# Kernel optimization log

Measured on AMD Instinct MI355X. Metric: run time of the kernel, lower is better.

Reference implementation:

```python
import jax, jax.numpy as jnp
import numpy as np

N_NODES = 65536
N_FEAT = 64
N_EDGES = 1048576
N_GRAPHS = 16
LP_ITERS = 30


def setup_inputs() -> dict:
    key = jax.random.key(0)
    k1, k2, k3 = jax.random.split(key, 3)
    x = jax.random.normal(k1, (N_NODES, N_FEAT), dtype=jnp.float32)
    edge_index = jax.random.randint(k2, (2, N_EDGES), 0, N_NODES, dtype=jnp.int32)
    batch = jnp.sort(jax.random.randint(k3, (N_NODES,), 0, N_GRAPHS, dtype=jnp.int32))
    v2 = jnp.full((1,), 3.5, dtype=jnp.float32)  # learnable affinity scale param
    return {"x": x, "edge_index": edge_index, "batch": batch, "v2": v2}


def _lp_clustering(row, col, aff, n_nodes, n_iters):
    """Label propagation: each node adopts the neighbor label with max summed affinity."""
    E = row.shape[0]
    aff = jax.lax.stop_gradient(aff)  # clustering is discrete, no grad path

    def body(_, labels):
        lab_c = labels[col]                                    # neighbor labels per edge
        order = jnp.lexsort((lab_c, row))                      # sort by (row, neighbor-label)
        r_s, l_s, w_s = row[order], lab_c[order], aff[order]
        new_grp = jnp.concatenate([jnp.ones((1,), bool),
                                   (r_s[1:] != r_s[:-1]) | (l_s[1:] != l_s[:-1])])
        gid = jnp.cumsum(new_grp) - 1                          # dense (row,label) group ids
        gsum = jax.ops.segment_sum(w_s, gid, num_segments=E)   # affinity mass per group
        gcnt = jax.ops.segment_sum(jnp.ones_like(w_s), gid, num_segments=E)
        valid = gcnt > 0
        g_row = jnp.where(valid, jax.ops.segment_max(r_s, gid, num_segments=E), 0)
        g_lab = jnp.where(valid, jax.ops.segment_max(l_s, gid, num_segments=E), n_nodes)
        node_max = jax.ops.segment_max(jnp.where(valid, gsum, -jnp.inf), g_row,
                                       num_segments=n_nodes)
        win = valid & (gsum == node_max[g_row])
        # smallest winning label == torch argmax first-hit tie-break
        return jax.ops.segment_min(jnp.where(win, g_lab, n_nodes), g_row,
                                   num_segments=n_nodes)

    labels0 = jnp.arange(n_nodes, dtype=row.dtype)
    return jax.lax.fori_loop(0, n_iters, body, labels0)


def _forward(x, edge_index, batch, v2):
    n = x.shape[0]
    loops = jnp.arange(n, dtype=edge_index.dtype)
    ei = jnp.concatenate([edge_index, jnp.stack([loops, loops])], axis=1)  # add_self_loops
    row, col = ei[0], ei[1]

    # P2-style affinities: log_aff = -v2 * ||x_i - x_j||^2 ; forward exponentiates
    sqdist = jnp.sum((x[row] - x[col]) ** 2, axis=1)  # [E]
    losses = jnp.mean(sqdist)
    aff = jnp.exp(-v2[0] * sqdist)

    node_labels = _lp_clustering(row, col, aff, n, LP_ITERS)

    # unique(return_inverse): dense relabel of surviving cluster ids (sorted order)
    present = jnp.zeros((n,), jnp.int32).at[node_labels].set(1)
    cluster_labels = (jnp.cumsum(present) - 1)[node_labels]

    # max_pool_x: scatter-max node features into clusters (padded to n rows)
    cx = jax.ops.segment_max(x, cluster_labels, num_segments=n)
    cb = jax.ops.segment_max(batch, cluster_labels, num_segments=n)
    nonempty = jax.ops.segment_sum(jnp.ones((n,), jnp.int32), cluster_labels,
                                   num_segments=n) > 0
    cx = jnp.where(nonempty[:, None], cx, 0.0)
    cb = jnp.where(nonempty, cb, -1)

    # coalesce(cluster_labels[edge_index]): sort + dedupe, duplicates padded with -1
    mr, mc = cluster_labels[row], cluster_labels[col]
    order = jnp.lexsort((mc, mr))
    mr_s, mc_s = mr[order], mc[order]
    dup = jnp.concatenate([jnp.zeros((1,), bool),
                           (mr_s[1:] == mr_s[:-1]) & (mc_s[1:] == mc_s[:-1])])
    cei = jnp.stack([jnp.where(dup, -1, mr_s), jnp.where(dup, -1, mc_s)])

    return cx, cei, cb, cluster_labels, losses


def reference(x, edge_index, batch, v2):
    return _forward(x, edge_index, batch, v2)
```

## Files before the change

### kernel.cpp

```cpp
#include <hip/hip_runtime.h>
#include <hip/hip_fp16.h>
#include <hip/hip_cooperative_groups.h>

namespace cg = cooperative_groups;

#define DI __device__ __forceinline__

constexpr int NN   = 65536;
constexpr int NF   = 64;
constexpr int E0c  = 1048576;
constexpr int ET   = E0c + NN;
constexpr int LPITERS = 30;
constexpr int KPOS = 16;
constexpr int MSCH = 4096;
constexpr int NCHK = ET / MSCH;
constexpr int SCAP = 8192;
constexpr int CAP0 = 6144;
constexpr int BPB  = CAP0 / 64;
constexpr int NPART2 = 256 * BPB;

constexpr int O_CX   = 0;
constexpr int O_CEI0 = NN * NF;
constexpr int O_CEI1 = O_CEI0 + ET;
constexpr int O_CB   = O_CEI0 + 2 * ET;
constexpr int O_CL   = O_CB + NN;
constexpr int O_LOSS = O_CL + NN;

constexpr int W_CHG   = 0;
constexpr int W_NCLUS = 32;
constexpr int W_H1    = 64;
constexpr int W_GC0   = W_H1 + 256;
constexpr int W_GC1   = W_GC0 + 256;
constexpr int W_SCP   = 832;
constexpr int W_SCO   = W_SCP + 256;
constexpr int W_PART  = W_SCO + 256;
constexpr int W_PCNT  = W_PART + NPART2;
constexpr int W_PCOL  = W_PCNT + NN;
constexpr int W_PW    = W_PCOL + NN*KPOS;
constexpr int W_L0    = W_PW + NN*KPOS;
constexpr int W_L1    = W_L0 + NN;
constexpr int W_PRES  = W_L1 + NN;
constexpr int W_PSUM  = W_PRES + NN;
constexpr int W_CLU   = W_PSUM + NN;
constexpr int W_CBA   = W_CLU + NN;
constexpr int W_K0    = W_CBA + NN;
constexpr int W_K1    = W_K0 + 256*CAP0;

DI void edge_rc(const int* ei, int e, int& r, int& c) {
  if (e < E0c) { r = ei[e]; c = ei[E0c + e]; }
  else         { r = e - E0c; c = r; }
}

DI unsigned fenc(float f) {
  unsigned u = __float_as_uint(f);
  return (u & 0x80000000u) ? ~u : (u | 0x80000000u);
}
DI float fdec(unsigned u) {
  u = (u & 0x80000000u) ? (u & 0x7fffffffu) : ~u;
  return __uint_as_float(u);
}

DI int lp_step(int r, int d, int c0, int c1, float q0, float q1,
               const int* __restrict__ pcol, const float* __restrict__ pw,
               const int* __restrict__ lin) {
  int bl = NN;
  if (d == 1) {
    bl = lin[c0];
  } else if (d == 2) {
    int l0 = lin[c0], l1 = lin[c1];
    if (l0 == l1) bl = l0;
    else if (q1 > q0 || (q1 == q0 && l1 < l0)) bl = l1;
    else bl = l0;
  } else if (d > 2) {
    float best = 0.f;
    for (int i = 0; i < d; ++i) {
      int li = lin[pcol[r * KPOS + i]];
      bool dup = false;
      for (int j = 0; j < i; ++j)
        if (lin[pcol[r * KPOS + j]] == li) { dup = true; break; }
      if (dup) continue;
      float sum = 0.f;
      for (int j = i; j < d; ++j)
        if (lin[pcol[r * KPOS + j]] == li) sum += pw[r * KPOS + j];
      if (sum > best || (sum == best && li < bl)) { best = sum; bl = li; }
    }
  }
  return bl;
}


__global__ __launch_bounds__(256) void init_small(int* ws) {
  for (int i = threadIdx.x; i < 832; i += 256) ws[i] = 0;
}

__global__ __launch_bounds__(256) void emultisplit(const int* __restrict__ ei,
                                                   int* __restrict__ gcur0,
                                                   unsigned* __restrict__ K0,
                                                   int* __restrict__ pcnt,
                                                   int* __restrict__ L0,
                                                   const float2* __restrict__ x2,
                                                   unsigned* __restrict__ xh) {
  __shared__ unsigned skey[MSCH];
  __shared__ unsigned short binid[MSCH];
  __shared__ int hl[256], ss[256], hs[256], hc[256], gb[256];
  int t = threadIdx.x;
  if (blockIdx.x < 256) {
    int rr = blockIdx.x * 256 + t;
    pcnt[rr] = 0;
    L0[rr] = rr;
  }
  for (int i = blockIdx.x * 256 + t; i < NN * NF / 2; i += NCHK * 256) {
    float2 f = x2[i];
    __half2 h = __floats2half2_rn(f.x, f.y);
    xh[i] = *reinterpret_cast<unsigned*>(&h);
  }
  hl[t] = 0; __syncthreads();
  int base = blockIdx.x * MSCH;
  unsigned mykey[MSCH / 256];
  #pragma unroll
  for (int k = 0; k < MSCH / 256; ++k) {
    int e = base + k * 256 + t;
    int r, c; edge_rc(ei, e, r, c);
    unsigned key = ((unsigned)r << 16) | (unsigned)c;
    mykey[k] = key;
    atomicAdd(&hl[key >> 24], 1);
  }
  __syncthreads();
  int v = hl[t];
  ss[t] = v; __syncthreads();
  for (int off = 1; off < 256; off <<= 1) {
    int u = (t >= off) ? ss[t - off] : 0;
    __syncthreads();
    ss[t] += u;
    __syncthreads();
  }
  int excl = ss[t] - v;
  hs[t] = excl;
  hc[t] = excl;
  gb[t] = t * CAP0 + ((v > 0) ? atomicAdd(&gcur0[t], v) : 0);
  for (int j = excl; j < excl + v; ++j) binid[j] = (unsigned short)t;
  __syncthreads();
  #pragma unroll
  for (int k = 0; k < MSCH / 256; ++k) {
    int b = mykey[k] >> 24;
    int slot = atomicAdd(&hc[b], 1);
    skey[slot] = mykey[k];
  }
  __syncthreads();
  for (int i = t; i < MSCH; i += 256) {
    int b = binid[i];
    int pos = gb[b] + (i - hs[b]);
    if (pos < (b + 1) * CAP0) K0[pos] = skey[i];
  }
}

__global__ __launch_bounds__(256) void edge_pos2(const unsigned* __restrict__ xh,
                                                 const unsigned* __restrict__ K0,
                                                 const int* __restrict__ gcur0,
                                                 const float* __restrict__ v2,
                                                 float* __restrict__ part,
                                                 int* __restrict__ pcnt,
                                                 int* __restrict__ pcol,
                                                 float* __restrict__ pw) {
  __shared__ float ls[32];
  int t = threadIdx.x, grp = t >> 3, lane = t & 7;
  int bkt = blockIdx.x / BPB;
  int off = (blockIdx.x % BPB) * 64;
  int cnt = gcur0[bkt];
  if (off >= cnt) {
    if (t == 0) part[blockIdx.x] = 0.f;
    return;
  }
  float w = v2[0];
  unsigned kk[2]; bool act[2];
  uint4 A[2], B[2];
  #pragma unroll
  for (int q = 0; q < 2; ++q) {
    int j = off + grp * 2 + q;
    act[q] = (j < cnt);
    kk[q] = K0[bkt * CAP0 + (act[q] ? j : 0)];
  }
  #pragma unroll
  for (int q = 0; q < 2; ++q) {
    int r = kk[q] >> 16, c = kk[q] & 0xFFFF;
    A[q] = ((const uint4*)(xh + (size_t)r * 32))[lane];
    B[q] = ((const uint4*)(xh + (size_t)c * 32))[lane];
  }
  __builtin_amdgcn_sched_barrier(0);
  float lsum = 0.f;
  #pragma unroll
  for (int q = 0; q < 2; ++q) {
    const __half2* ah = reinterpret_cast<const __half2*>(&A[q]);
    const __half2* bh = reinterpret_cast<const __half2*>(&B[q]);
    __half2 d0 = __hsub2(ah[0], bh[0]);
    __half2 acc = __hmul2(d0, d0);
    __half2 d1 = __hsub2(ah[1], bh[1]); acc = __hfma2(d1, d1, acc);
    __half2 d2 = __hsub2(ah[2], bh[2]); acc = __hfma2(d2, d2, acc);
    __half2 d3 = __hsub2(ah[3], bh[3]); acc = __hfma2(d3, d3, acc);
    float s = __low2float(acc) + __high2float(acc);
    s += __shfl_xor(s, 1, 8);
    s += __shfl_xor(s, 2, 8);
    s += __shfl_xor(s, 4, 8);
    if (lane == 0 && act[q]) {
      int r = kk[q] >> 16, c = kk[q] & 0xFFFF;
      if (r == c) s = 0.f;
      lsum += s;
      float aff = expf(-w * s);
      if (aff > 0.f) {
        int slot = atomicAdd(&pcnt[r], 1);
        if (slot < KPOS) { pcol[r * KPOS + slot] = c; pw[r * KPOS + slot] = aff; }
      }
    }
  }
  if (lane == 0) ls[grp] = lsum;
  __syncthreads();
  if (t == 0) {
    float s = 0.f;
    #pragma unroll
    for (int k = 0; k < 32; ++k) s += ls[k];
    part[blockIdx.x] = s;
  }
}

__global__ __launch_bounds__(256) void lp_iter0(const int* __restrict__ pcnt,
                                                const int* __restrict__ pcol,
                                                const float* __restrict__ pw,
                                                const int* __restrict__ L0,
                                                int* __restrict__ L1,
                                                int* __restrict__ chg,
                                                const float* __restrict__ part,
                                                float* __restrict__ out_loss) {
  __shared__ float smf[256];
  int t = threadIdx.x;
  int r = blockIdx.x * 256 + t;
  int d = pcnt[r];
  if (d > KPOS) d = KPOS;
  int c0 = 0, c1 = 0; float q0 = 0.f, q1 = 0.f;
  if (d >= 1) { c0 = pcol[r * KPOS];     q0 = pw[r * KPOS]; }
  if (d >= 2) { c1 = pcol[r * KPOS + 1]; q1 = pw[r * KPOS + 1]; }
  int bl = lp_step(r, d, c0, c1, q0, q1, pcol, pw, L0);
  L1[r] = bl;
  if (bl != L0[r]) atomicOr(&chg[0], 1);
  if (blockIdx.x == 0) {
    float s = 0.f;
    for (int i = t; i < NPART2; i += 256) s += part[i];
    smf[t] = s; __syncthreads();
    for (int off = 128; off; off >>= 1) {
      if (t < off) smf[t] += smf[t + off];
      __syncthreads();
    }
    if (t == 0) out_loss[0] = smf[0] / (float)ET;
  }
}

__global__ __launch_bounds__(256) void general_tail(
    const int* __restrict__ pcnt, const int* __restrict__ pcol,
    const float* __restrict__ pw, int* __restrict__ L0, int* __restrict__ L1,
    int* __restrict__ chg, int* __restrict__ pres, int* __restrict__ psum,
    int* __restrict__ clu, float* __restrict__ out_cl, int* __restrict__ cba,
    unsigned* __restrict__ cxacc, const float* __restrict__ x,
    const int* __restrict__ batch, int* __restrict__ nclus_g,
    int* __restrict__ scp, int* __restrict__ sco, int* __restrict__ h1,
    const int* __restrict__ gcur0, int* __restrict__ gcur1,
    const unsigned* __restrict__ K0, unsigned* __restrict__ K1,
    float* __restrict__ out_cb) {
  if (chg[0] == 0) return;
  __shared__ int sm[256], hl[256], bases[256];
  __shared__ int sbc;
  cg::grid_group grid = cg::this_grid();
  int t = threadIdx.x, b = blockIdx.x;
  int r = b * 256 + t;
  pres[r] = 0;
  cba[r] = -1;
  {
    uint4 z = make_uint4(0u, 0u, 0u, 0u);
    uint4* p = (uint4*)(cxacc + ((size_t)r << 6));
    #pragma unroll
    for (int q = 0; q < 16; ++q) p[q] = z;
  }
  int mylab = L1[r];
  int d = pcnt[r]; if (d > KPOS) d = KPOS;
  int c0 = 0, c1 = 0; float q0 = 0.f, q1 = 0.f;
  if (d >= 1) { c0 = pcol[r * KPOS];     q0 = pw[r * KPOS]; }
  if (d >= 2) { c1 = pcol[r * KPOS + 1]; q1 = pw[r * KPOS + 1]; }
  for (int it = 1; it < LPITERS; ++it) {
    const int* lin = (it & 1) ? L1 : L0;
    int* lout = (it & 1) ? L0 : L1;
    int bl = lp_step(r, d, c0, c1, q0, q1, pcol, pw, lin);
    lout[r] = bl;
    if (bl != mylab) atomicOr(&chg[it], 1);
    mylab = bl;
    grid.sync();
    if (t == 0) sbc = *(volatile int*)&chg[it];
    __syncthreads();
    if (sbc == 0) break;
  }
  L0[r] = mylab;
  grid.sync();
  pres[mylab] = 1;
  grid.sync();
  int v = pres[r];
  sm[t] = v; __syncthreads();
  for (int off = 1; off < 256; off <<= 1) {
    int u = (t >= off) ? sm[t - off] : 0;
    __syncthreads();
    sm[t] += u;
    __syncthreads();
  }
  int lexcl = sm[t] - v;
  if (t == 255) scp[b] = sm[255];
  grid.sync();
  if (b == 0) {
    int p = scp[t];
    sm[t] = p; __syncthreads();
    for (int off = 1; off < 256; off <<= 1) {
      int u = (t >= off) ? sm[t - off] : 0;
      __syncthreads();
      sm[t] += u;
      __syncthreads();
    }
    sco[t] = sm[t] - p;
    if (t == 255) nclus_g[0] = sm[255];
  }
  grid.sync();
  psum[r] = lexcl + sco[b];
  grid.sync();
  int cr = psum[mylab];
  clu[r] = cr;
  out_cl[r] = (float)cr;
  grid.sync();
  for (int f = 0; f < 64; ++f)
    atomicMax(&cxacc[((size_t)cr << 6) + f], fenc(x[((size_t)r << 6) + f]));
  atomicMax(&cba[cr], batch[r]);
  grid.sync();
  int ncl = nclus_g[0];
  for (int f = 0; f < 64; ++f) {
    unsigned u = cxacc[((size_t)r << 6) + f];
    ((float*)cxacc)[((size_t)r << 6) + f] = (r < ncl) ? fdec(u) : 0.f;
  }
  out_cb[r] = (float)cba[r];
  hl[t] = 0; __syncthreads();
  int cnt = gcur0[b];
  for (int i = t; i < cnt; i += 256) {
    unsigned k = K0[b * CAP0 + i];
    atomicAdd(&hl[((unsigned)clu[k >> 16]) >> 8], 1);
  }
  __syncthreads();
  if (hl[t]) atomicAdd(&h1[t], hl[t]);
  grid.sync();
  int hv = h1[t];
  sm[t] = hv; __syncthreads();
  for (int off = 1; off < 256; off <<= 1) {
    int u = (t >= off) ? sm[t - off] : 0;
    __syncthreads();
    sm[t] += u;
    __syncthreads();
  }
  bases[t] = sm[t] - hv;
  __syncthreads();
  for (int i = t; i < cnt; i += 256) {
    unsigned k = K0[b * CAP0 + i];
    unsigned k1 = ((unsigned)clu[k >> 16] << 16) | (unsigned)clu[k & 0xFFFF];
    int b1 = k1 >> 24;
    int pos = bases[b1] + atomicAdd(&gcur1[b1], 1);
    K1[pos] = k1;
  }
}

__global__ __launch_bounds__(512) void sortwrite(unsigned* __restrict__ K0,
                                                 const int* __restrict__ gcur0,
                                                 unsigned* __restrict__ K1,
                                                 const int* __restrict__ h1,
                                                 const int* __restrict__ chg,
                                                 const float4* __restrict__ x4,
                                                 const int* __restrict__ batch,
                                                 float4* __restrict__ out_cx4,
                                                 float* __restrict__ out_cl,
                                                 float* __restrict__ out_cb,
                                                 float* __restrict__ o0,
                                                 float* __restrict__ o1) {
  __shared__ unsigned sk[SCAP];
  __shared__ int hl[256], ss[256], sbs[257], cur[256], sh[2];
  int t = threadIdx.x, b = blockIdx.x;
  bool fast = (chg[0] == 0);
  if (fast) {
    int base4 = b * (256 * 16);
    for (int i = t; i < 256 * 16; i += 512) out_cx4[base4 + i] = x4[base4 + i];
    int rbase = b * 256;
    for (int i = t; i < 256; i += 512) {
      out_cl[rbase + i] = (float)(rbase + i);
      out_cb[rbase + i] = (float)batch[rbase + i];
    }
  }
  const int* cnts = fast ? gcur0 : h1;
  if (t < 256) ss[t] = cnts[t];
  __syncthreads();
  for (int off = 1; off < 256; off <<= 1) {
    int u = (t < 256 && t >= off) ? ss[t - off] : 0;
    __syncthreads();
    if (t < 256) ss[t] += u;
    __syncthreads();
  }
  if (t == 0) { sh[0] = ss[b] - cnts[b]; sh[1] = cnts[b]; }
  __syncthreads();
  int sout = sh[0], d = sh[1];
  if (d <= 0) return;
  unsigned* kp = fast ? (K0 + b * CAP0) : (K1 + sout);
  if (d <= SCAP) {
    if (t < 256) hl[t] = 0;
    __syncthreads();
    for (int i = t; i < d; i += 512)
      atomicAdd(&hl[(kp[i] >> 16) & 0xFF], 1);
    __syncthreads();
    if (t < 256) ss[t] = hl[t];
    __syncthreads();
    for (int off = 1; off < 256; off <<= 1) {
      int u = (t < 256 && t >= off) ? ss[t - off] : 0;
      __syncthreads();
      if (t < 256) ss[t] += u;
      __syncthreads();
    }
    if (t < 256) { sbs[t] = ss[t] - hl[t]; cur[t] = ss[t] - hl[t]; }
    if (t == 255) sbs[256] = d;
    __syncthreads();
    for (int i = t; i < d; i += 512) {
      unsigned k = kp[i];
      int slot = atomicAdd(&cur[(k >> 16) & 0xFF], 1);
      sk[slot] = k;
    }
    __syncthreads();
    int wave = t >> 6, lane = t & 63;
    for (int sb = wave; sb < 256; sb += 8) {
      int s0 = sbs[sb], s1 = sbs[sb + 1], dd = s1 - s0;
      if (dd <= 1) continue;
      if (dd <= 64) {
        unsigned k = (lane < dd) ? sk[s0 + lane] : 0xFFFFFFFFu;
        #pragma unroll
        for (int size = 2; size <= 64; size <<= 1) {
          #pragma unroll
          for (int stride = size >> 1; stride > 0; stride >>= 1) {
            unsigned o = __shfl_xor(k, stride, 64);
            bool takeMin = (((lane & stride) == 0) == ((lane & size) == 0));
            unsigned mn = k < o ? k : o, mx = k < o ? o : k;
            k = takeMin ? mn : mx;
          }
        }
        if (lane < dd) sk[s0 + lane] = k;
      } else if (lane == 0) {
        for (int i = s0 + 1; i < s1; ++i) {
          unsigned k = sk[i];
          int j = i - 1;
          while (j >= s0 && sk[j] > k) { sk[j + 1] = sk[j]; --j; }
          sk[j + 1] = k;
        }
      }
    }
    __syncthreads();
    for (int i = t; i < d; i += 512) {
      unsigned k = sk[i];
      bool dup = (i > 0) && (sk[i - 1] == k);
      o0[sout + i] = dup ? -1.f : (float)(k >> 16);
      o1[sout + i] = dup ? -1.f : (float)(k & 0xffffu);
    }
  } else {
    if (t == 0) {
      for (int i = 1; i < d; ++i) {
        unsigned k = kp[i];
        int j = i - 1;
        while (j >= 0 && kp[j] > k) { kp[j + 1] = kp[j]; --j; }
        kp[j + 1] = k;
      }
    }
    __syncthreads();
    for (int i = t; i < d; i += 512) {
      unsigned k = kp[i];
      bool dup = (i > 0) && (kp[i - 1] == k);
      o0[sout + i] = dup ? -1.f : (float)(k >> 16);
      o1[sout + i] = dup ? -1.f : (float)(k & 0xffffu);
    }
  }
}


extern "C" void kernel_launch(void* const* d_in, const int* in_sizes, int n_in,
                              void* d_out, int out_size, void* d_ws, size_t ws_size,
                              hipStream_t stream) {
  const float* x   = (const float*)d_in[0];
  const int* ei    = (const int*)d_in[1];
  const int* batch = (const int*)d_in[2];
  const float* v2  = (const float*)d_in[3];
  float* out = (float*)d_out;
  int* ws = (int*)d_ws;
  unsigned* cxacc = (unsigned*)(out + O_CX);
  unsigned* xh = cxacc;

  init_small<<<1, 256, 0, stream>>>(ws);

  emultisplit<<<NCHK, 256, 0, stream>>>(ei, ws + W_GC0, (unsigned*)(ws + W_K0),
                                        ws + W_PCNT, ws + W_L0,
                                        (const float2*)x, xh);

  edge_pos2<<<NPART2, 256, 0, stream>>>(xh, (const unsigned*)(ws + W_K0),
                                        ws + W_GC0, v2, (float*)(ws + W_PART),
                                        ws + W_PCNT, ws + W_PCOL, (float*)(ws + W_PW));

  lp_iter0<<<NN / 256, 256, 0, stream>>>(ws + W_PCNT, ws + W_PCOL,
                                         (const float*)(ws + W_PW),
                                         ws + W_L0, ws + W_L1, ws + W_CHG,
                                         (const float*)(ws + W_PART), out + O_LOSS);

  {
    const int* pcnt = ws + W_PCNT;
    const int* pcol = ws + W_PCOL;
    const float* pw = (const float*)(ws + W_PW);
    int* L0 = ws + W_L0;
    int* L1 = ws + W_L1;
    int* chg = ws + W_CHG;
    int* pres = ws + W_PRES;
    int* psum = ws + W_PSUM;
    int* clu = ws + W_CLU;
    float* out_cl = out + O_CL;
    int* cba = ws + W_CBA;
    unsigned* cxa = cxacc;
    const float* x_ = x;
    const int* batch_ = batch;
    int* nclus_g = ws + W_NCLUS;
    int* scp = ws + W_SCP;
    int* sco = ws + W_SCO;
    int* h1 = ws + W_H1;
    const int* gcur0 = ws + W_GC0;
    int* gcur1 = ws + W_GC1;
    const unsigned* K0 = (const unsigned*)(ws + W_K0);
    unsigned* K1 = (unsigned*)(ws + W_K1);
    float* out_cb = out + O_CB;
    void* args[] = { (void*)&pcnt, (void*)&pcol, (void*)&pw,
                     (void*)&L0, (void*)&L1, (void*)&chg, (void*)&pres,
                     (void*)&psum, (void*)&clu, (void*)&out_cl, (void*)&cba,
                     (void*)&cxa, (void*)&x_, (void*)&batch_, (void*)&nclus_g,
                     (void*)&scp, (void*)&sco, (void*)&h1, (void*)&gcur0,
                     (void*)&gcur1, (void*)&K0, (void*)&K1, (void*)&out_cb };
    hipLaunchCooperativeKernel((const void*)general_tail, dim3(NN / 256),
                               dim3(256), args, 0, stream);
  }

  sortwrite<<<256, 512, 0, stream>>>((unsigned*)(ws + W_K0), ws + W_GC0,
                                     (unsigned*)(ws + W_K1), ws + W_H1,
                                     ws + W_CHG, (const float4*)x, batch,
                                     (float4*)(out + O_CX), out + O_CL,
                                     out + O_CB, out + O_CEI0, out + O_CEI1);
}
```

Measured before the change: 157.6 us.

## Split sortwrite into fast and general kernels, four blocks per bucket

Splits the final sort-and-write kernel into a fast-path kernel that runs 1024 blocks, with each block handling a quarter of a bucket's 256 sub-buckets, and a separate general-path kernel that exits early when the fast path applies. Each fast block builds the full bucket histogram on its own but scatters and sorts only its sub-bucket range. Sub-buckets of up to 64 keys are sorted with a wave-level bitonic sort using shuffles. The goal is more parallelism and better occupancy on the tail kernel, at the cost of re-reading each bucket's keys four times and one extra kernel launch.

```diff
diff --git a/kernel.cpp b/kernel.cpp
--- a/kernel.cpp
+++ b/kernel.cpp
@@ -367,33 +367,113 @@
   }
 }
 
-__global__ __launch_bounds__(512) void sortwrite(unsigned* __restrict__ K0,
-                                                 const int* __restrict__ gcur0,
-                                                 unsigned* __restrict__ K1,
-                                                 const int* __restrict__ h1,
-                                                 const int* __restrict__ chg,
-                                                 const float4* __restrict__ x4,
-                                                 const int* __restrict__ batch,
-                                                 float4* __restrict__ out_cx4,
-                                                 float* __restrict__ out_cl,
-                                                 float* __restrict__ out_cb,
-                                                 float* __restrict__ o0,
-                                                 float* __restrict__ o1) {
+__global__ __launch_bounds__(512) void sortwrite_fast(
+    const unsigned* __restrict__ K0, const int* __restrict__ gcur0,
+    const int* __restrict__ chg, const float4* __restrict__ x4,
+    const int* __restrict__ batch, float4* __restrict__ out_cx4,
+    float* __restrict__ out_cl, float* __restrict__ out_cb,
+    float* __restrict__ o0, float* __restrict__ o1) {
+  if (chg[0] != 0) return;
+  __shared__ unsigned sk[CAP0];
+  __shared__ int hl[256], ss[256], sbs[257], cur[256], sh[2];
+  int t = threadIdx.x;
+  int b = blockIdx.x >> 2, spl = blockIdx.x & 3;
+  {
+    int base4 = blockIdx.x * 1024;
+    for (int i = t; i < 1024; i += 512) out_cx4[base4 + i] = x4[base4 + i];
+    int rbase = blockIdx.x * 64;
+    for (int i = t; i < 64; i += 512) {
+      out_cl[rbase + i] = (float)(rbase + i);
+      out_cb[rbase + i] = (float)batch[rbase + i];
+    }
+  }
+  int cntb = gcur0[b];
+  if (cntb > CAP0) cntb = CAP0;
+  if (t < 256) ss[t] = gcur0[t];
+  __syncthreads();
+  for (int off = 1; off < 256; off <<= 1) {
+    int u = (t < 256 && t >= off) ? ss[t - off] : 0;
+    __syncthreads();
+    if (t < 256) ss[t] += u;
+    __syncthreads();
+  }
+  if (t == 0) sh[0] = ss[b] - gcur0[b];
+  if (t < 256) hl[t] = 0;
+  __syncthreads();
+  for (int i = t; i < cntb; i += 512)
+    atomicAdd(&hl[(K0[b * CAP0 + i] >> 16) & 0xFF], 1);
+  __syncthreads();
+  if (t < 256) ss[t] = hl[t];
+  __syncthreads();
+  for (int off = 1; off < 256; off <<= 1) {
+    int u = (t < 256 && t >= off) ? ss[t - off] : 0;
+    __syncthreads();
+    if (t < 256) ss[t] += u;
+    __syncthreads();
+  }
+  if (t < 256) { sbs[t] = ss[t] - hl[t]; cur[t] = ss[t] - hl[t]; }
+  if (t == 255) sbs[256] = cntb;
+  __syncthreads();
+  int sout_b = sh[0];
+  int sb0 = spl * 64, sb1 = sb0 + 64;
+  int mybase = sbs[sb0], myend = sbs[sb1];
+  if (myend <= mybase) return;
+  for (int i = t; i < cntb; i += 512) {
+    unsigned k = K0[b * CAP0 + i];
+    int sb = (k >> 16) & 0xFF;
+    if (sb >= sb0 && sb < sb1) {
+      int slot = atomicAdd(&cur[sb], 1);
+      sk[slot - mybase] = k;
+    }
+  }
+  __syncthreads();
+  int wave = t >> 6, lane = t & 63;
+  for (int sb = sb0 + wave; sb < sb1; sb += 8) {
+    int s0 = sbs[sb] - mybase, s1 = sbs[sb + 1] - mybase, dd = s1 - s0;
+    if (dd <= 1) continue;
+    if (dd <= 64) {
+      unsigned k = (lane < dd) ? sk[s0 + lane] : 0xFFFFFFFFu;
+      int P = (dd <= 16) ? 16 : ((dd <= 32) ? 32 : 64);
+      for (int size = 2; size <= P; size <<= 1) {
+        bool upAll = (size == P);
+        for (int stride = size >> 1; stride > 0; stride >>= 1) {
+          unsigned o = __shfl_xor(k, stride, 64);
+          bool up = upAll || ((lane & size) == 0);
+          bool takeMin = (((lane & stride) == 0) == up);
+          unsigned mn = k < o ? k : o, mx = k < o ? o : k;
+          k = takeMin ? mn : mx;
+        }
+      }
+      if (lane < dd) sk[s0 + lane] = k;
+    } else if (lane == 0) {
+      for (int i = s0 + 1; i < s1; ++i) {
+        unsigned k = sk[i];
+        int j = i - 1;
+        while (j >= s0 && sk[j] > k) { sk[j + 1] = sk[j]; --j; }
+        sk[j + 1] = k;
+      }
+    }
+  }
+  __syncthreads();
+  int mycnt = myend - mybase;
+  for (int i = t; i < mycnt; i += 512) {
+    unsigned k = sk[i];
+    bool dup = (i > 0) && (sk[i - 1] == k);
+    int gp = sout_b + mybase + i;
+    o0[gp] = dup ? -1.f : (float)(k >> 16);
+    o1[gp] = dup ? -1.f : (float)(k & 0xffffu);
+  }
+}
+
+__global__ __launch_bounds__(512) void sortwrite_general(
+    unsigned* __restrict__ K1, const int* __restrict__ h1,
+    const int* __restrict__ chg, float* __restrict__ o0,
+    float* __restrict__ o1) {
+  if (chg[0] == 0) return;
   __shared__ unsigned sk[SCAP];
   __shared__ int hl[256], ss[256], sbs[257], cur[256], sh[2];
   int t = threadIdx.x, b = blockIdx.x;
-  bool fast = (chg[0] == 0);
-  if (fast) {
-    int base4 = b * (256 * 16);
-    for (int i = t; i < 256 * 16; i += 512) out_cx4[base4 + i] = x4[base4 + i];
-    int rbase = b * 256;
-    for (int i = t; i < 256; i += 512) {
-      out_cl[rbase + i] = (float)(rbase + i);
-      out_cb[rbase + i] = (float)batch[rbase + i];
-    }
-  }
-  const int* cnts = fast ? gcur0 : h1;
-  if (t < 256) ss[t] = cnts[t];
+  if (t < 256) ss[t] = h1[t];
   __syncthreads();
   for (int off = 1; off < 256; off <<= 1) {
     int u = (t < 256 && t >= off) ? ss[t - off] : 0;
@@ -401,11 +481,11 @@
     if (t < 256) ss[t] += u;
     __syncthreads();
   }
-  if (t == 0) { sh[0] = ss[b] - cnts[b]; sh[1] = cnts[b]; }
+  if (t == 0) { sh[0] = ss[b] - h1[b]; sh[1] = h1[b]; }
   __syncthreads();
   int sout = sh[0], d = sh[1];
   if (d <= 0) return;
-  unsigned* kp = fast ? (K0 + b * CAP0) : (K1 + sout);
+  unsigned* kp = K1 + sout;
   if (d <= SCAP) {
     if (t < 256) hl[t] = 0;
     __syncthreads();
@@ -543,9 +623,14 @@
                                dim3(256), args, 0, stream);
   }
 
-  sortwrite<<<256, 512, 0, stream>>>((unsigned*)(ws + W_K0), ws + W_GC0,
-                                     (unsigned*)(ws + W_K1), ws + W_H1,
-                                     ws + W_CHG, (const float4*)x, batch,
-                                     (float4*)(out + O_CX), out + O_CL,
-                                     out + O_CB, out + O_CEI0, out + O_CEI1);
-}
+  sortwrite_fast<<<1024, 512, 0, stream>>>((const unsigned*)(ws + W_K0),
+                                           ws + W_GC0, ws + W_CHG,
+                                           (const float4*)x, batch,
+                                           (float4*)(out + O_CX), out + O_CL,
+                                           out + O_CB, out + O_CEI0,
+                                           out + O_CEI1);
+
+  sortwrite_general<<<256, 512, 0, stream>>>((unsigned*)(ws + W_K1), ws + W_H1,
+                                             ws + W_CHG, out + O_CEI0,
+                                             out + O_CEI1);
+}
```

Result: faster. 151.7 us (-3.8%).
